# Performance work log

Measured on AMD Instinct MI355X. Metric: run time of the kernel, lower is better.

Reference implementation:

```python
import jax, jax.numpy as jnp
import numpy as np

N = 100000          # nodes
E = 1_600_000       # edges (before self loops)
IN = 128            # in_channels
HID = 64            # hidden
HEADS = 4
EPS = 1e-5          # BatchNorm eps
NEG_SLOPE = 0.2     # GATConv leaky_relu slope


def setup_inputs() -> dict:
    key = jax.random.key(0)
    ks = jax.random.split(key, 16)
    he = lambda fan: (2.0 / fan) ** 0.5  # kaiming-normal scale
    d = {
        "x": jax.random.normal(ks[0], (N, IN), jnp.float32),
        "edge_index": jax.random.randint(ks[1], (2, E), 0, N, dtype=jnp.int64),
        "root_index": 0,
        "W1": jax.random.normal(ks[2], (IN, HEADS * HID), jnp.float32) * he(IN),
        "att_src1": jax.random.normal(ks[3], (HEADS, HID), jnp.float32) * 0.1,
        "att_dst1": jax.random.normal(ks[4], (HEADS, HID), jnp.float32) * 0.1,
        "b1": jnp.zeros((HEADS * HID,), jnp.float32),
        "W2": jax.random.normal(ks[5], (HEADS * HID, HID), jnp.float32) * he(HEADS * HID),
        "att_src2": jax.random.normal(ks[6], (1, HID), jnp.float32) * 0.1,
        "att_dst2": jax.random.normal(ks[7], (1, HID), jnp.float32) * 0.1,
        "b2": jnp.zeros((HID,), jnp.float32),
        "bn1_g": jnp.ones((HEADS * HID,), jnp.float32),
        "bn1_b": jnp.zeros((HEADS * HID,), jnp.float32),
        "bn1_m": jnp.zeros((HEADS * HID,), jnp.float32),
        "bn1_v": jnp.ones((HEADS * HID,), jnp.float32),
        "bn2_g": jnp.ones((HID,), jnp.float32),
        "bn2_b": jnp.zeros((HID,), jnp.float32),
        "bn2_m": jnp.zeros((HID,), jnp.float32),
        "bn2_v": jnp.ones((HID,), jnp.float32),
        "cg1_w": jax.random.normal(ks[8], (3 * HID, 64), jnp.float32) * he(3 * HID),
        "cg1_b": jnp.zeros((64,), jnp.float32),
        "cbn_g": jnp.ones((64,), jnp.float32),
        "cbn_b": jnp.zeros((64,), jnp.float32),
        "cbn_m": jnp.zeros((64,), jnp.float32),
        "cbn_v": jnp.ones((64,), jnp.float32),
        "cg2_w": jax.random.normal(ks[9], (64, 32), jnp.float32) * he(64),
        "cg2_b": jnp.zeros((32,), jnp.float32),
        "cg3_w": jax.random.normal(ks[10], (32, 1), jnp.float32) * he(32),
        "cg3_b": jnp.zeros((1,), jnp.float32),
    }
    return d


def _bn_eval(x, g, b, m, v):
    return (x - m) * jax.lax.rsqrt(v + EPS) * g + b


def _gat_conv(x, src, dst, W, att_src, att_dst, bias, heads, out_ch, concat):
    """PyG GATConv (eval mode, self loops already in src/dst)."""
    n = x.shape[0]
    h = (x @ W).reshape(n, heads, out_ch)                # [N,H,C]
    a_src = jnp.einsum('nhc,hc->nh', h, att_src)         # [N,H]
    a_dst = jnp.einsum('nhc,hc->nh', h, att_dst)
    e = jax.nn.leaky_relu(a_src[src] + a_dst[dst], NEG_SLOPE)   # [Etot,H]
    seg_max = jax.ops.segment_max(e, dst, num_segments=n)
    ex = jnp.exp(e - seg_max[dst])
    denom = jax.ops.segment_sum(ex, dst, num_segments=n)
    alpha = ex / (denom[dst] + 1e-16)                    # [Etot,H]
    msg = h[src] * alpha[:, :, None]                     # [Etot,H,C]
    out = jax.ops.segment_sum(msg, dst, num_segments=n)  # [N,H,C]
    if concat:
        return out.reshape(n, heads * out_ch) + bias
    return out.mean(axis=1) + bias


def reference(x, edge_index, root_index, W1, att_src1, att_dst1, b1,
              W2, att_src2, att_dst2, b2,
              bn1_g, bn1_b, bn1_m, bn1_v, bn2_g, bn2_b, bn2_m, bn2_v,
              cg1_w, cg1_b, cbn_g, cbn_b, cbn_m, cbn_v,
              cg2_w, cg2_b, cg3_w, cg3_b):
    n = x.shape[0]
    # add self loops (PyG GATConv default)
    loop = jnp.arange(n, dtype=edge_index.dtype)
    src = jnp.concatenate([edge_index[0], loop])
    dst = jnp.concatenate([edge_index[1], loop])

    h = _gat_conv(x, src, dst, W1, att_src1, att_dst1, b1, HEADS, HID, True)
    h = jax.nn.elu(_bn_eval(h, bn1_g, bn1_b, bn1_m, bn1_v))
    h = _gat_conv(h, src, dst, W2, att_src2, att_dst2, b2, 1, HID, False)
    node_emb = jax.nn.elu(_bn_eval(h, bn2_g, bn2_b, bn2_m, bn2_v))  # [N,HID]

    mean_emb = node_emb.mean(axis=0, keepdims=True)      # [1,HID]
    max_emb = node_emb.max(axis=0, keepdims=True)        # [1,HID]
    safe_root = min(root_index, n - 1)
    root_emb = node_emb[safe_root][None, :]              # single graph path
    g = jnp.concatenate([mean_emb, max_emb, root_emb], axis=-1)  # [1,3*HID]

    g = jax.nn.relu(_bn_eval(g @ cg1_w + cg1_b, cbn_g, cbn_b, cbn_m, cbn_v))
    g = jax.nn.relu(g @ cg2_w + cg2_b)
    logit = (g @ cg3_w + cg3_b).squeeze(-1)              # [1]
    return logit
```

## Files before the change

kernel.cpp:

```cpp
#include <hip/hip_runtime.h>

#define N_NODES 100000
#define N_EDGES 1600000
#define ETOT    1700000
#define IN_CH   128
#define C1      256
#define HID     64
#define BN_EPS  1e-5f
#define SLOPE   0.2f
#define NCHUNK  98

typedef __attribute__((ext_vector_type(8))) short s16x8;
typedef __attribute__((ext_vector_type(4))) float f32x4;
#define MFMA16(a, b, c) __builtin_amdgcn_mfma_f32_16x16x32_bf16(a, b, c, 0, 0, 0)

__device__ __forceinline__ float leaky(float x) { return fmaxf(x, SLOPE * x); }
__device__ __forceinline__ float elu_f(float x) { return x > 0.f ? x : __expf(x) - 1.f; }
__device__ __forceinline__ unsigned short f2bf(float f) {
  unsigned int b = __float_as_uint(f);
  return (unsigned short)((b + 0x7FFFu + ((b >> 16) & 1u)) >> 16);
}
__device__ __forceinline__ float bf2f(unsigned short u) {
  return __uint_as_float((unsigned int)u << 16);
}

__global__ void __launch_bounds__(256) k_init_deg(int* __restrict__ deg) {
  int n = blockIdx.x * 256 + threadIdx.x;
  if (n < N_NODES) deg[n] = 1;
}

__global__ void __launch_bounds__(256) k_deg(const int* __restrict__ edge, int* __restrict__ deg) {
  int i = blockIdx.x * 256 + threadIdx.x;
  if (i < N_EDGES) atomicAdd(&deg[edge[N_EDGES + i]], 1);
}

__global__ void __launch_bounds__(256) k_scan_part(const int* __restrict__ deg, int* __restrict__ part) {
  __shared__ int ls[256];
  int t = threadIdx.x;
  int base = blockIdx.x * 1024 + t * 4;
  int s = 0;
#pragma unroll
  for (int j = 0; j < 4; j++) if (base + j < N_NODES) s += deg[base + j];
  ls[t] = s;
  __syncthreads();
  for (int off = 128; off >= 1; off >>= 1) {
    if (t < off) ls[t] += ls[t + off];
    __syncthreads();
  }
  if (t == 0) part[blockIdx.x] = ls[0];
}

__global__ void k_scan_top(int* __restrict__ part, int* __restrict__ row_ptr) {
  if (threadIdx.x == 0 && blockIdx.x == 0) {
    int run = 0;
    for (int i = 0; i < NCHUNK; i++) { int t = part[i]; part[i] = run; run += t; }
    row_ptr[N_NODES] = run;
  }
}

__global__ void __launch_bounds__(256) k_scan_down(const int* __restrict__ deg, const int* __restrict__ part,
                                                   int* __restrict__ row_ptr, int* __restrict__ cursor) {
  __shared__ int ls[256];
  int t = threadIdx.x;
  int base = blockIdx.x * 1024 + t * 4;
  int v[4];
#pragma unroll
  for (int j = 0; j < 4; j++) v[j] = (base + j < N_NODES) ? deg[base + j] : 0;
  int tsum = v[0] + v[1] + v[2] + v[3];
  ls[t] = tsum;
  __syncthreads();
  for (int off = 1; off < 256; off <<= 1) {
    int add = (t >= off) ? ls[t - off] : 0;
    __syncthreads();
    ls[t] += add;
    __syncthreads();
  }
  int excl = ls[t] - tsum + part[blockIdx.x];
#pragma unroll
  for (int j = 0; j < 4; j++) {
    int idx = base + j;
    if (idx < N_NODES) { row_ptr[idx] = excl; cursor[idx] = excl; }
    excl += v[j];
  }
}

__global__ void __launch_bounds__(256) k_fill(const int* __restrict__ edge, int* __restrict__ cursor,
                                              int* __restrict__ col) {
  int i = blockIdx.x * 256 + threadIdx.x;
  int s, d;
  if (i < N_EDGES) { s = edge[i]; d = edge[N_EDGES + i]; }
  else if (i < ETOT) { s = i - N_EDGES; d = s; }
  else return;
  int pos = atomicAdd(&cursor[d], 1);
  col[pos] = s;
}

__global__ void __launch_bounds__(256) k_prep(const float* __restrict__ W1, const float* __restrict__ W2,
                                              unsigned short* __restrict__ W1T, unsigned short* __restrict__ W2T) {
  int i = blockIdx.x * 256 + threadIdx.x;
  if (i < IN_CH * C1) {
    int k = i >> 8, c = i & 255;
    W1T[c * IN_CH + k] = f2bf(W1[i]);
  }
  if (i < C1 * HID) {
    int k = i >> 6, c = i & 63;
    W2T[c * C1 + k] = f2bf(W2[i]);
  }
}

__global__ void __launch_bounds__(256) k_gemm1(const float* __restrict__ x, const unsigned short* __restrict__ W1T,
                                               const float* __restrict__ attS, const float* __restrict__ attD,
                                               unsigned short* __restrict__ h1b, float* __restrict__ aS,
                                               float* __restrict__ aD) {
  __shared__ unsigned short As[64][IN_CH + 8];
  int tid = threadIdx.x;
  int w = tid >> 6, lane = tid & 63;
  int l15 = lane & 15, l4 = lane >> 4;
  int row0 = blockIdx.x * 64;
#pragma unroll
  for (int it = 0; it < 8; it++) {
    int idx = tid + it * 256;
    int r = idx >> 5;
    int k4 = (idx & 31) * 4;
    int gr = row0 + r; if (gr >= N_NODES) gr = N_NODES - 1;
    float4 v = *(const float4*)(x + (size_t)gr * IN_CH + k4);
    ushort4 bvec;
    bvec.x = f2bf(v.x); bvec.y = f2bf(v.y); bvec.z = f2bf(v.z); bvec.w = f2bf(v.w);
    *(ushort4*)&As[r][k4] = bvec;
  }
  __syncthreads();
  f32x4 acc[4][4];
#pragma unroll
  for (int mf = 0; mf < 4; mf++)
#pragma unroll
    for (int cf = 0; cf < 4; cf++) acc[mf][cf] = (f32x4){0.f, 0.f, 0.f, 0.f};
#pragma unroll
  for (int ks = 0; ks < 4; ks++) {
    int koff = ks * 32 + l4 * 8;
    s16x8 a[4];
#pragma unroll
    for (int mf = 0; mf < 4; mf++) a[mf] = *(const s16x8*)&As[mf * 16 + l15][koff];
#pragma unroll
    for (int cf = 0; cf < 4; cf++) {
      s16x8 b = *(const s16x8*)(W1T + (size_t)(w * 64 + cf * 16 + l15) * IN_CH + koff);
#pragma unroll
      for (int mf = 0; mf < 4; mf++) acc[mf][cf] = MFMA16(a[mf], b, acc[mf][cf]);
    }
  }
  float as_c[4], ad_c[4];
#pragma unroll
  for (int cf = 0; cf < 4; cf++) {
    as_c[cf] = attS[w * HID + cf * 16 + l15];
    ad_c[cf] = attD[w * HID + cf * 16 + l15];
  }
#pragma unroll
  for (int mf = 0; mf < 4; mf++) {
#pragma unroll
    for (int reg = 0; reg < 4; reg++) {
      int gr = row0 + mf * 16 + l4 * 4 + reg;
      bool ok = gr < N_NODES;
      float s = 0.f, dd = 0.f;
#pragma unroll
      for (int cf = 0; cf < 4; cf++) {
        float v = acc[mf][cf][reg];
        if (ok) h1b[(size_t)gr * C1 + w * 64 + cf * 16 + l15] = f2bf(v);
        s += v * as_c[cf];
        dd += v * ad_c[cf];
      }
#pragma unroll
      for (int m = 1; m <= 8; m <<= 1) { s += __shfl_xor(s, m, 64); dd += __shfl_xor(dd, m, 64); }
      if (ok && l15 == 0) {
        aS[(size_t)gr * 4 + w] = s;
        aD[(size_t)gr * 4 + w] = dd;
      }
    }
  }
}

__global__ void __launch_bounds__(256) k_agg1(const int* __restrict__ row_ptr, const int* __restrict__ col,
                                              const float* __restrict__ aS, const float* __restrict__ aD,
                                              const unsigned short* __restrict__ h1b, const float* __restrict__ b1,
                                              const float* __restrict__ g1, const float* __restrict__ be1,
                                              const float* __restrict__ m1, const float* __restrict__ v1,
                                              unsigned short* __restrict__ hmb) {
  int wave = threadIdx.x >> 6;
  int lane = threadIdx.x & 63;
  int d = blockIdx.x * 4 + wave;
  if (d >= N_NODES) return;
  int head = lane >> 4;
  float ad = aD[d * 4 + head];
  int s0 = row_ptr[d], s1 = row_ptr[d + 1];
  float denom = 0.f;
  float4 acc = {0.f, 0.f, 0.f, 0.f};
  int c0 = lane * 4;
  int i = s0;
  int iend8 = s0 + ((s1 - s0) & ~7);
  for (; i < iend8; i += 8) {
    int cv = col[i + (lane & 7)];
    int sid[8];
#pragma unroll
    for (int j = 0; j < 8; j++) sid[j] = __builtin_amdgcn_readfirstlane(__shfl(cv, j));
    float e[8];
#pragma unroll
    for (int j = 0; j < 8; j++) e[j] = aS[(sid[j] << 2) + head];
    ushort4 h[8];
#pragma unroll
    for (int j = 0; j < 8; j++) h[j] = *(const ushort4*)(h1b + ((size_t)sid[j] << 8) + c0);
    float wv[8];
#pragma unroll
    for (int j = 0; j < 8; j++) wv[j] = __expf(fminf(leaky(e[j] + ad), 80.f));
#pragma unroll
    for (int j = 0; j < 8; j++) {
      denom += wv[j];
      acc.x += wv[j] * bf2f(h[j].x);
      acc.y += wv[j] * bf2f(h[j].y);
      acc.z += wv[j] * bf2f(h[j].z);
      acc.w += wv[j] * bf2f(h[j].w);
    }
  }
  for (; i < s1; i++) {
    int s = __builtin_amdgcn_readfirstlane(col[i]);
    float e = aS[(s << 2) + head];
    ushort4 hv = *(const ushort4*)(h1b + ((size_t)s << 8) + c0);
    float wv = __expf(fminf(leaky(e + ad), 80.f));
    denom += wv;
    acc.x += wv * bf2f(hv.x);
    acc.y += wv * bf2f(hv.y);
    acc.z += wv * bf2f(hv.z);
    acc.w += wv * bf2f(hv.w);
  }
  float inv = 1.f / (denom + 1e-16f);
  float4 bb = *(const float4*)(b1 + c0);
  float4 gg = *(const float4*)(g1 + c0);
  float4 be = *(const float4*)(be1 + c0);
  float4 mm = *(const float4*)(m1 + c0);
  float4 vv = *(const float4*)(v1 + c0);
  ushort4 o;
  o.x = f2bf(elu_f((acc.x * inv + bb.x - mm.x) * rsqrtf(vv.x + BN_EPS) * gg.x + be.x));
  o.y = f2bf(elu_f((acc.y * inv + bb.y - mm.y) * rsqrtf(vv.y + BN_EPS) * gg.y + be.y));
  o.z = f2bf(elu_f((acc.z * inv + bb.z - mm.z) * rsqrtf(vv.z + BN_EPS) * gg.z + be.z));
  o.w = f2bf(elu_f((acc.w * inv + bb.w - mm.w) * rsqrtf(vv.w + BN_EPS) * gg.w + be.w));
  *(ushort4*)(hmb + (size_t)d * C1 + c0) = o;
}

__global__ void __launch_bounds__(256) k_gemm2(const unsigned short* __restrict__ hmb, const unsigned short* __restrict__ W2T,
                                               const float* __restrict__ attS, const float* __restrict__ attD,
                                               unsigned short* __restrict__ h2b, float* __restrict__ aS,
                                               float* __restrict__ aD) {
  __shared__ unsigned short As[64][C1 + 8];
  int tid = threadIdx.x;
  int w = tid >> 6, lane = tid & 63;
  int l15 = lane & 15, l4 = lane >> 4;
  int row0 = blockIdx.x * 64;
#pragma unroll
  for (int it = 0; it < 8; it++) {
    int idx = tid + it * 256;
    int r = idx >> 5;
    int k8 = (idx & 31) * 8;
    int gr = row0 + r; if (gr >= N_NODES) gr = N_NODES - 1;
    *(uint4*)&As[r][k8] = *(const uint4*)(hmb + (size_t)gr * C1 + k8);
  }
  __syncthreads();
  f32x4 acc[4];
#pragma unroll
  for (int cf = 0; cf < 4; cf++) acc[cf] = (f32x4){0.f, 0.f, 0.f, 0.f};
#pragma unroll
  for (int ks = 0; ks < 8; ks++) {
    int koff = ks * 32 + l4 * 8;
    s16x8 a = *(const s16x8*)&As[w * 16 + l15][koff];
#pragma unroll
    for (int cf = 0; cf < 4; cf++) {
      s16x8 b = *(const s16x8*)(W2T + (size_t)(cf * 16 + l15) * C1 + koff);
      acc[cf] = MFMA16(a, b, acc[cf]);
    }
  }
  float as_c[4], ad_c[4];
#pragma unroll
  for (int cf = 0; cf < 4; cf++) {
    as_c[cf] = attS[cf * 16 + l15];
    ad_c[cf] = attD[cf * 16 + l15];
  }
#pragma unroll
  for (int reg = 0; reg < 4; reg++) {
    int gr = row0 + w * 16 + l4 * 4 + reg;
    bool ok = gr < N_NODES;
    float s = 0.f, dd = 0.f;
#pragma unroll
    for (int cf = 0; cf < 4; cf++) {
      float v = acc[cf][reg];
      if (ok) h2b[(size_t)gr * HID + cf * 16 + l15] = f2bf(v);
      s += v * as_c[cf];
      dd += v * ad_c[cf];
    }
#pragma unroll
    for (int m = 1; m <= 8; m <<= 1) { s += __shfl_xor(s, m, 64); dd += __shfl_xor(dd, m, 64); }
    if (ok && l15 == 0) { aS[gr] = s; aD[gr] = dd; }
  }
}

__global__ void __launch_bounds__(256) k_agg2(const int* __restrict__ row_ptr, const int* __restrict__ col,
                                              const float* __restrict__ aS, const float* __restrict__ aD,
                                              const unsigned short* __restrict__ h2b, const float* __restrict__ b2,
                                              const float* __restrict__ g2, const float* __restrict__ be2,
                                              const float* __restrict__ m2, const float* __restrict__ v2,
                                              float* __restrict__ emb) {
  int wave = threadIdx.x >> 6;
  int lane = threadIdx.x & 63;
  int d = blockIdx.x * 4 + wave;
  if (d >= N_NODES) return;
  float ad = aD[d];
  int s0 = row_ptr[d], s1 = row_ptr[d + 1];
  float denom = 0.f, acc = 0.f;
  int i = s0;
  int iend8 = s0 + ((s1 - s0) & ~7);
  for (; i < iend8; i += 8) {
    int cv = col[i + (lane & 7)];
    int sid[8];
#pragma unroll
    for (int j = 0; j < 8; j++) sid[j] = __builtin_amdgcn_readfirstlane(__shfl(cv, j));
    float e[8];
#pragma unroll
    for (int j = 0; j < 8; j++) e[j] = aS[sid[j]];
    unsigned short h[8];
#pragma unroll
    for (int j = 0; j < 8; j++) h[j] = h2b[((size_t)sid[j] << 6) + lane];
    float wv[8];
#pragma unroll
    for (int j = 0; j < 8; j++) wv[j] = __expf(fminf(leaky(e[j] + ad), 80.f));
#pragma unroll
    for (int j = 0; j < 8; j++) {
      denom += wv[j];
      acc += wv[j] * bf2f(h[j]);
    }
  }
  for (; i < s1; i++) {
    int s = __builtin_amdgcn_readfirstlane(col[i]);
    float e = aS[s];
    unsigned short hv = h2b[((size_t)s << 6) + lane];
    float wv = __expf(fminf(leaky(e + ad), 80.f));
    denom += wv;
    acc += wv * bf2f(hv);
  }
  float o = acc / (denom + 1e-16f) + b2[lane];
  o = (o - m2[lane]) * rsqrtf(v2[lane] + BN_EPS) * g2[lane] + be2[lane];
  emb[(size_t)d * HID + lane] = elu_f(o);
}

__global__ void __launch_bounds__(256) k_pool(const float* __restrict__ emb, float* __restrict__ psum,
                                              float* __restrict__ pmax) {
  __shared__ float ss[4][64], sm[4][64];
  int t = threadIdx.x;
  int c = t & 63, rg = t >> 6;
  float s = 0.f, m = -INFINITY;
  for (int n = blockIdx.x * 4 + rg; n < N_NODES; n += gridDim.x * 4) {
    float v = emb[(size_t)n * HID + c];
    s += v; m = fmaxf(m, v);
  }
  ss[rg][c] = s; sm[rg][c] = m;
  __syncthreads();
  if (t < 64) {
    psum[blockIdx.x * 64 + t] = ss[0][t] + ss[1][t] + ss[2][t] + ss[3][t];
    pmax[blockIdx.x * 64 + t] = fmaxf(fmaxf(sm[0][t], sm[1][t]), fmaxf(sm[2][t], sm[3][t]));
  }
}

__global__ void __launch_bounds__(256) k_final(const float* __restrict__ psum, const float* __restrict__ pmax,
                                               const float* __restrict__ emb, const int* __restrict__ rootp,
                                               const float* __restrict__ cg1w, const float* __restrict__ cg1b,
                                               const float* __restrict__ cbng, const float* __restrict__ cbnb,
                                               const float* __restrict__ cbnm, const float* __restrict__ cbnv,
                                               const float* __restrict__ cg2w, const float* __restrict__ cg2b,
                                               const float* __restrict__ cg3w, const float* __restrict__ cg3b,
                                               float* __restrict__ out) {
  __shared__ float ss[4][64], sm[4][64];
  __shared__ float g[192], t1[64], t2[32];
  int t = threadIdx.x;
  int c = t & 63, q = t >> 6;
  float s = 0.f, m = -INFINITY;
  for (int b = q; b < 256; b += 4) {
    s += psum[b * 64 + c];
    m = fmaxf(m, pmax[b * 64 + c]);
  }
  ss[q][c] = s; sm[q][c] = m;
  __syncthreads();
  if (t < 64) {
    float tot = ss[0][t] + ss[1][t] + ss[2][t] + ss[3][t];
    float mx = fmaxf(fmaxf(sm[0][t], sm[1][t]), fmaxf(sm[2][t], sm[3][t]));
    int root = rootp[0];
    if (root > N_NODES - 1) root = N_NODES - 1;
    if (root < 0) root = 0;
    g[t] = tot / (float)N_NODES;
    g[64 + t] = mx;
    g[128 + t] = emb[(size_t)root * HID + t];
  }
  __syncthreads();
  if (t < 64) {
    float o = cg1b[t];
    for (int i = 0; i < 192; i++) o += g[i] * cg1w[i * 64 + t];
    o = (o - cbnm[t]) * rsqrtf(cbnv[t] + BN_EPS) * cbng[t] + cbnb[t];
    t1[t] = o > 0.f ? o : 0.f;
  }
  __syncthreads();
  if (t < 32) {
    float o = cg2b[t];
    for (int i = 0; i < 64; i++) o += t1[i] * cg2w[i * 32 + t];
    t2[t] = o > 0.f ? o : 0.f;
  }
  __syncthreads();
  if (t == 0) {
    float o = cg3b[0];
    for (int i = 0; i < 32; i++) o += t2[i] * cg3w[i];
    out[0] = o;
  }
}

extern "C" void kernel_launch(void* const* d_in, const int* in_sizes, int n_in,
                              void* d_out, int out_size, void* d_ws, size_t ws_size,
                              hipStream_t stream) {
  const float* x     = (const float*)d_in[0];
  const int*   edge  = (const int*)d_in[1];
  const int*   root  = (const int*)d_in[2];
  const float* W1    = (const float*)d_in[3];
  const float* attS1 = (const float*)d_in[4];
  const float* attD1 = (const float*)d_in[5];
  const float* b1    = (const float*)d_in[6];
  const float* W2    = (const float*)d_in[7];
  const float* attS2 = (const float*)d_in[8];
  const float* attD2 = (const float*)d_in[9];
  const float* b2    = (const float*)d_in[10];
  const float* bn1g  = (const float*)d_in[11];
  const float* bn1b  = (const float*)d_in[12];
  const float* bn1m  = (const float*)d_in[13];
  const float* bn1v  = (const float*)d_in[14];
  const float* bn2g  = (const float*)d_in[15];
  const float* bn2b  = (const float*)d_in[16];
  const float* bn2m  = (const float*)d_in[17];
  const float* bn2v  = (const float*)d_in[18];
  const float* cg1w  = (const float*)d_in[19];
  const float* cg1b  = (const float*)d_in[20];
  const float* cbng  = (const float*)d_in[21];
  const float* cbnb  = (const float*)d_in[22];
  const float* cbnm  = (const float*)d_in[23];
  const float* cbnv  = (const float*)d_in[24];
  const float* cg2w  = (const float*)d_in[25];
  const float* cg2b  = (const float*)d_in[26];
  const float* cg3w  = (const float*)d_in[27];
  const float* cg3b  = (const float*)d_in[28];

  char* ws = (char*)d_ws;
  size_t off = 0;
  auto carve = [&](size_t bytes) { char* p = ws + off; off += (bytes + 255) & ~(size_t)255; return p; };
  unsigned short* h1b = (unsigned short*)carve((size_t)N_NODES * C1 * 2);
  unsigned short* hmb = (unsigned short*)carve((size_t)N_NODES * C1 * 2);
  float* aS1     = (float*)carve((size_t)N_NODES * 4 * 4);
  float* aD1     = (float*)carve((size_t)N_NODES * 4 * 4);
  int*   deg     = (int*)  carve((size_t)N_NODES * 4);
  int*   row_ptr = (int*)  carve((size_t)(N_NODES + 1) * 4);
  int*   cursor  = (int*)  carve((size_t)N_NODES * 4);
  int*   col     = (int*)  carve((size_t)ETOT * 4);
  int*   part    = (int*)  carve(512);
  unsigned short* W1T = (unsigned short*)carve((size_t)IN_CH * C1 * 2);
  unsigned short* W2T = (unsigned short*)carve((size_t)C1 * HID * 2);
  unsigned short* h2b = h1b;
  float* aS2  = (float*)(h1b + (size_t)N_NODES * HID);
  float* aD2  = aS2 + N_NODES;
  float* emb  = (float*)hmb;
  float* psum = emb + (size_t)N_NODES * HID;
  float* pmax = psum + 256 * 64;

  k_init_deg<<<(N_NODES + 255) / 256, 256, 0, stream>>>(deg);
  k_deg<<<(N_EDGES + 255) / 256, 256, 0, stream>>>(edge, deg);
  k_prep<<<(IN_CH * C1 + 255) / 256, 256, 0, stream>>>(W1, W2, W1T, W2T);
  k_scan_part<<<NCHUNK, 256, 0, stream>>>(deg, part);
  k_scan_top<<<1, 64, 0, stream>>>(part, row_ptr);
  k_scan_down<<<NCHUNK, 256, 0, stream>>>(deg, part, row_ptr, cursor);
  k_fill<<<(ETOT + 255) / 256, 256, 0, stream>>>(edge, cursor, col);
  k_gemm1<<<(N_NODES + 63) / 64, 256, 0, stream>>>(x, W1T, attS1, attD1, h1b, aS1, aD1);
  k_agg1<<<(N_NODES + 3) / 4, 256, 0, stream>>>(row_ptr, col, aS1, aD1, h1b, b1, bn1g, bn1b, bn1m, bn1v, hmb);
  k_gemm2<<<(N_NODES + 63) / 64, 256, 0, stream>>>(hmb, W2T, attS2, attD2, h2b, aS2, aD2);
  k_agg2<<<(N_NODES + 3) / 4, 256, 0, stream>>>(row_ptr, col, aS2, aD2, h2b, b2, bn2g, bn2b, bn2m, bn2v, emb);
  k_pool<<<256, 256, 0, stream>>>(emb, psum, pmax);
  k_final<<<1, 256, 0, stream>>>(psum, pmax, emb, root, cg1w, cg1b, cbng, cbnb, cbnm, cbnv,
                                 cg2w, cg2b, cg3w, cg3b, (float*)d_out);
}
```

Baseline: 548.7 us.

## Partition degree count and CSR fill into destination-range phases

Degree counting and CSR fill are split into 8 phases, each handling only the destinations in a 12500-node range. Every phase rescans the full edge list but issues atomics only for its range, so the atomic targets (cursor/deg, and col writes) stay within a cache-friendly window. The degree kernel also moves to int4 vectorized loads. The trade is reading the edge array 8 times and launching 8x more blocks, in exchange for better locality of the scattered atomics and writes.

```diff
diff --git a/kernel.cpp b/kernel.cpp
--- a/kernel.cpp
+++ b/kernel.cpp
@@ -9,6 +9,8 @@
 #define BN_EPS  1e-5f
 #define SLOPE   0.2f
 #define NCHUNK  98
+#define FILL_PH 8
+#define PH_NODES 12500
 
 typedef __attribute__((ext_vector_type(8))) short s16x8;
 typedef __attribute__((ext_vector_type(4))) float f32x4;
@@ -29,9 +31,24 @@
   if (n < N_NODES) deg[n] = 1;
 }
 
-__global__ void __launch_bounds__(256) k_deg(const int* __restrict__ edge, int* __restrict__ deg) {
-  int i = blockIdx.x * 256 + threadIdx.x;
-  if (i < N_EDGES) atomicAdd(&deg[edge[N_EDGES + i]], 1);
+__global__ void __launch_bounds__(256) k_deg_ph(const int* __restrict__ edge, int* __restrict__ deg) {
+  int bpp = (N_EDGES + 1023) >> 10;
+  int ph = blockIdx.x / bpp;
+  int lo = ph * PH_NODES, hi = lo + PH_NODES;
+  int i0 = (blockIdx.x % bpp) * 1024 + threadIdx.x * 4;
+  if (i0 >= N_EDGES) return;
+  if (i0 + 3 < N_EDGES) {
+    int4 dv = *(const int4*)(edge + N_EDGES + i0);
+    if (dv.x >= lo && dv.x < hi) atomicAdd(&deg[dv.x], 1);
+    if (dv.y >= lo && dv.y < hi) atomicAdd(&deg[dv.y], 1);
+    if (dv.z >= lo && dv.z < hi) atomicAdd(&deg[dv.z], 1);
+    if (dv.w >= lo && dv.w < hi) atomicAdd(&deg[dv.w], 1);
+  } else {
+    for (int j = 0; j < 4 && i0 + j < N_EDGES; j++) {
+      int d = edge[N_EDGES + i0 + j];
+      if (d >= lo && d < hi) atomicAdd(&deg[d], 1);
+    }
+  }
 }
 
 __global__ void __launch_bounds__(256) k_scan_part(const int* __restrict__ deg, int* __restrict__ part) {
@@ -84,13 +101,16 @@
   }
 }
 
-__global__ void __launch_bounds__(256) k_fill(const int* __restrict__ edge, int* __restrict__ cursor,
-                                              int* __restrict__ col) {
-  int i = blockIdx.x * 256 + threadIdx.x;
-  int s, d;
-  if (i < N_EDGES) { s = edge[i]; d = edge[N_EDGES + i]; }
-  else if (i < ETOT) { s = i - N_EDGES; d = s; }
-  else return;
+__global__ void __launch_bounds__(256) k_fill_ph(const int* __restrict__ edge, int* __restrict__ cursor,
+                                                 int* __restrict__ col) {
+  int bpp = (ETOT + 255) >> 8;
+  int ph = blockIdx.x / bpp;
+  int lo = ph * PH_NODES, hi = lo + PH_NODES;
+  int i = (blockIdx.x % bpp) * 256 + threadIdx.x;
+  if (i >= ETOT) return;
+  int d = (i < N_EDGES) ? edge[N_EDGES + i] : (i - N_EDGES);
+  if (d < lo || d >= hi) return;
+  int s = (i < N_EDGES) ? edge[i] : d;
   int pos = atomicAdd(&cursor[d], 1);
   col[pos] = s;
 }
@@ -468,13 +488,15 @@
   float* psum = emb + (size_t)N_NODES * HID;
   float* pmax = psum + 256 * 64;
 
+  int bpp_deg  = (N_EDGES + 1023) >> 10;
+  int bpp_fill = (ETOT + 255) >> 8;
   k_init_deg<<<(N_NODES + 255) / 256, 256, 0, stream>>>(deg);
-  k_deg<<<(N_EDGES + 255) / 256, 256, 0, stream>>>(edge, deg);
+  k_deg_ph<<<bpp_deg * FILL_PH, 256, 0, stream>>>(edge, deg);
   k_prep<<<(IN_CH * C1 + 255) / 256, 256, 0, stream>>>(W1, W2, W1T, W2T);
   k_scan_part<<<NCHUNK, 256, 0, stream>>>(deg, part);
   k_scan_top<<<1, 64, 0, stream>>>(part, row_ptr);
   k_scan_down<<<NCHUNK, 256, 0, stream>>>(deg, part, row_ptr, cursor);
-  k_fill<<<(ETOT + 255) / 256, 256, 0, stream>>>(edge, cursor, col);
+  k_fill_ph<<<bpp_fill * FILL_PH, 256, 0, stream>>>(edge, cursor, col);
   k_gemm1<<<(N_NODES + 63) / 64, 256, 0, stream>>>(x, W1T, attS1, attD1, h1b, aS1, aD1);
   k_agg1<<<(N_NODES + 3) / 4, 256, 0, stream>>>(row_ptr, col, aS1, aD1, h1b, b1, bn1g, bn1b, bn1m, bn1v, hmb);
   k_gemm2<<<(N_NODES + 63) / 64, 256, 0, stream>>>(hmb, W2T, attS2, attD2, h2b, aS2, aD2);
```

Result: faster. 502.9 us (-8.3%).
